# Kernel tuning notes

Measured on AMD Instinct MI355X. Metric: run time of the kernel, lower is better.

## Reference

```python
import jax, jax.numpy as jnp
import numpy as np

EMBED_DIM = 2048
HEAD_DIM = 128
BLOCK = 2048
BATCH = 8


def setup_inputs() -> dict:
    key = jax.random.key(0)
    kx, kq, kk, kv = jax.random.split(key, 4)
    x = jax.random.normal(kx, (BATCH, BLOCK, EMBED_DIM), dtype=jnp.float32)
    # torch nn.Linear(embed_dim, head_dim, bias=False) weight shape: [head_dim, embed_dim]
    s = 1.0 / np.sqrt(EMBED_DIM)
    Wq = jax.random.uniform(kq, (HEAD_DIM, EMBED_DIM), jnp.float32, -s, s)
    Wk = jax.random.uniform(kk, (HEAD_DIM, EMBED_DIM), jnp.float32, -s, s)
    Wv = jax.random.uniform(kv, (HEAD_DIM, EMBED_DIM), jnp.float32, -s, s)
    return {"x": x, "Wq": Wq, "Wk": Wk, "Wv": Wv}


def reference(x, Wq, Wk, Wv):
    B, T, C = x.shape
    # projections: y = x @ W.T
    q = jnp.einsum('btc,hc->bth', x, Wq)   # [B,T,H]
    k = jnp.einsum('btc,hc->bth', x, Wk)
    v = jnp.einsum('btc,hc->bth', x, Wv)
    # NOTE: original scales by embed_dim**0.5, not head_dim**0.5
    scale = 1.0 / jnp.sqrt(jnp.float32(C))
    logits = jnp.einsum('bth,bsh->bts', q, k) * scale  # [B,T,T]
    # causal mask (is_decoder=True)
    causal = jnp.tril(jnp.ones((T, T), dtype=bool))
    logits = jnp.where(causal, logits, -jnp.inf)
    weights = jax.nn.softmax(logits, axis=-1)
    attention = jnp.einsum('bts,bsh->bth', weights, v)  # [B,T,H]
    return attention
```

## Files before the change

### kernel.cpp

```cpp
#include <hip/hip_runtime.h>
#include <hip/hip_bf16.h>
#include <stdint.h>

constexpr int B    = 8;
constexpr int T    = 2048;
constexpr int EMB  = 2048;
constexpr int HD   = 128;
constexpr int M    = B * T;
constexpr int NW   = 3 * HD;

typedef __attribute__((ext_vector_type(8))) short short8;
typedef __attribute__((ext_vector_type(4))) float f32x4;

__device__ inline unsigned short f2bf(float f) {
    union { float f; unsigned int u; } v; v.f = f;
    unsigned int x = v.u;
    unsigned int r = (x + 0x7FFFu + ((x >> 16) & 1u)) >> 16;
    return (unsigned short)r;
}

__device__ inline unsigned int cvt_pk_bf16(float a, float b) {
    unsigned int r;
    asm volatile("v_cvt_pk_bf16_f32 %0, %1, %2" : "=v"(r) : "v"(a), "v"(b));
    return r;
}

__global__ __launch_bounds__(256) void conv_w(
    const float* __restrict__ Wq, const float* __restrict__ Wk, const float* __restrict__ Wv,
    unsigned short* __restrict__ Wb)
{
    int base = (blockIdx.x * 256 + threadIdx.x) * 8;
    int row = base >> 11, col = base & 2047;
    const float* src;
    if (row < 128)      src = Wq + (size_t)row * EMB + col;
    else if (row < 256) src = Wk + (size_t)(row - 128) * EMB + col;
    else                src = Wv + (size_t)(row - 256) * EMB + col;
    float4 a = *(const float4*)src;
    float4 b = *(const float4*)(src + 4);
    short8 sv;
    sv[0] = f2bf(a.x); sv[1] = f2bf(a.y); sv[2] = f2bf(a.z); sv[3] = f2bf(a.w);
    sv[4] = f2bf(b.x); sv[5] = f2bf(b.y); sv[6] = f2bf(b.z); sv[7] = f2bf(b.w);
    *(short8*)(Wb + base) = sv;
}

constexpr int PBM = 64;
constexpr int PBN = 192;
constexpr int PBK = 64;
constexpr int PNT = EMB / PBK;

__global__ __launch_bounds__(256, 2) void qkv_proj(
    const float* __restrict__ x, const unsigned short* __restrict__ Wb,
    unsigned short* __restrict__ Qb, unsigned short* __restrict__ Kb,
    unsigned short* __restrict__ VtG)
{
    __shared__ unsigned short Ab[2][PBM * PBK];
    __shared__ unsigned short Bb[2][PBN * PBK];

    const int d   = blockIdx.x;
    const int xcd = d & 7;
    const int g   = d >> 3;
    const int mt  = xcd * 32 + (g >> 1);
    const int ns  = g & 1;
    const int m0  = mt * PBM;
    const int n0  = ns * PBN;
    const int phase = g & 31;

    const int tid  = threadIdx.x;
    const int lane = tid & 63;
    const int w    = tid >> 6;
    const int lo   = lane & 15;
    const int hi   = lane >> 4;

    const int ar = tid >> 2;
    const int s0 = (tid & 3) * 2;
    const float* asrc = x + (size_t)(m0 + ar) * EMB + s0 * 8;

    f32x4 acc[4][3];
#pragma unroll
    for (int i = 0; i < 4; ++i)
#pragma unroll
        for (int j = 0; j < 3; ++j) acc[i][j] = (f32x4)0.0f;

    short8 breg[6];
    float4 a0, a1, a2, a3;

    auto loadTile = [&](int k0) {
#pragma unroll
        for (int it = 0; it < 6; ++it) {
            int c = it * 256 + tid;
            int row = c >> 3, seg = c & 7;
            breg[it] = *(const short8*)(Wb + (size_t)(n0 + row) * EMB + k0 + seg * 8);
        }
        a0 = *(const float4*)(asrc + k0);
        a1 = *(const float4*)(asrc + k0 + 4);
        a2 = *(const float4*)(asrc + k0 + 8);
        a3 = *(const float4*)(asrc + k0 + 12);
    };
    auto writeTile = [&](int buf) {
#pragma unroll
        for (int it = 0; it < 6; ++it) {
            int c = it * 256 + tid;
            int row = c >> 3, seg = c & 7;
            *(short8*)&Bb[buf][row * PBK + (seg ^ (row & 7)) * 8] = breg[it];
        }
        uint4 p0, p1;
        p0.x = cvt_pk_bf16(a0.x, a0.y);  p0.y = cvt_pk_bf16(a0.z, a0.w);
        p0.z = cvt_pk_bf16(a1.x, a1.y);  p0.w = cvt_pk_bf16(a1.z, a1.w);
        p1.x = cvt_pk_bf16(a2.x, a2.y);  p1.y = cvt_pk_bf16(a2.z, a2.w);
        p1.z = cvt_pk_bf16(a3.x, a3.y);  p1.w = cvt_pk_bf16(a3.z, a3.w);
        *(uint4*)&Ab[buf][ar * PBK + ((s0    ) ^ (ar & 7)) * 8] = p0;
        *(uint4*)&Ab[buf][ar * PBK + ((s0 + 1) ^ (ar & 7)) * 8] = p1;
    };
    auto compute = [&](int buf) {
#pragma unroll
        for (int kk = 0; kk < 2; ++kk) {
            short8 af[4], bf[3];
            const int cseg = kk * 4 + hi;
#pragma unroll
            for (int i = 0; i < 4; ++i) {
                int R = i * 16 + lo;
                af[i] = *(const short8*)&Ab[buf][R * PBK + (cseg ^ (R & 7)) * 8];
            }
#pragma unroll
            for (int j = 0; j < 3; ++j) {
                int n = w * 48 + j * 16 + lo;
                bf[j] = *(const short8*)&Bb[buf][n * PBK + (cseg ^ (n & 7)) * 8];
            }
#pragma unroll
            for (int i = 0; i < 4; ++i)
#pragma unroll
                for (int j = 0; j < 3; ++j)
                    acc[i][j] = __builtin_amdgcn_mfma_f32_16x16x32_bf16(af[i], bf[j], acc[i][j], 0, 0, 0);
        }
    };

    loadTile(phase * PBK);
    writeTile(0);
    __syncthreads();

#pragma unroll 1
    for (int t = 0; t < PNT; ++t) {
        const int buf = t & 1;
        if (t + 1 < PNT) {
            const int tnext = (phase + t + 1) & 31;
            loadTile(tnext * PBK);
            __builtin_amdgcn_sched_barrier(0);
        }
        compute(buf);
        if (t + 1 < PNT) {
            __builtin_amdgcn_sched_barrier(0);
            writeTile(buf ^ 1);
            __syncthreads();
        }
    }

    const int b = m0 >> 11;
#pragma unroll
    for (int i = 0; i < 4; ++i) {
        int mrow0 = m0 + i * 16 + hi * 4;
#pragma unroll
        for (int j = 0; j < 3; ++j) {
            int colbase = n0 + w * 48 + j * 16 + lo;
            if (colbase < 128) {
#pragma unroll
                for (int r = 0; r < 4; ++r)
                    Qb[(size_t)(mrow0 + r) * HD + colbase] = f2bf(acc[i][j][r]);
            } else if (colbase < 256) {
#pragma unroll
                for (int r = 0; r < 4; ++r)
                    Kb[(size_t)(mrow0 + r) * HD + (colbase - 128)] = f2bf(acc[i][j][r]);
            } else {
                int h = colbase - 256;
                int tloc = mrow0 - b * T;
                ushort4 pv;
                pv.x = f2bf(acc[i][j][0]); pv.y = f2bf(acc[i][j][1]);
                pv.z = f2bf(acc[i][j][2]); pv.w = f2bf(acc[i][j][3]);
                *(ushort4*)(VtG + ((size_t)(b * HD + h)) * T + tloc) = pv;
            }
        }
    }
}

constexpr int QB = 64;
constexpr int KB = 64;
constexpr int STILES = 8;

__global__ __launch_bounds__(256) void attn_fwd(
    const unsigned short* __restrict__ Qb,
    const unsigned short* __restrict__ Kb,
    const unsigned short* __restrict__ VtG,
    float* __restrict__ out,
    float* __restrict__ part_o, float* __restrict__ part_ml,
    int use_split)
{
    const int b  = blockIdx.y;
    int bx = blockIdx.x;
    int qt, s, nsplit;
    if (use_split) {
        if (bx < 8)       { qt = bx;               s = 0; }
        else if (bx < 24) { qt = 8  + (bx - 8) / 2;  s = (bx - 8) & 1; }
        else if (bx < 48) { qt = 16 + (bx - 24) / 3; s = (bx - 24) % 3; }
        else              { qt = 24 + (bx - 48) / 4; s = (bx - 48) & 3; }
        nsplit = qt / 8 + 1;
    } else {
        qt = bx; s = 0; nsplit = 1;
    }
    const int q0 = qt * QB;
    int t0 = s * STILES;
    int t1 = t0 + STILES; if (t1 > qt + 1) t1 = qt + 1;

    const int tid  = threadIdx.x;
    const int lane = tid & 63;
    const int w    = tid >> 6;
    const int lo   = lane & 15;
    const int hi   = lane >> 4;

    __shared__ unsigned short Ks[KB][HD + 8];
    __shared__ unsigned short Vt[HD][KB + 16];
    __shared__ unsigned short Ps[QB][KB + 8];

    short8 qf[4];
    {
        int row = q0 + w * 16 + lo;
        const unsigned short* qp = Qb + ((size_t)b * T + row) * HD + hi * 8;
#pragma unroll
        for (int ks = 0; ks < 4; ++ks) qf[ks] = *(const short8*)(qp + ks * 32);
    }

    float mrow[4], lrow[4];
    f32x4 o[8];
#pragma unroll
    for (int r = 0; r < 4; ++r) { mrow[r] = -1e30f; lrow[r] = 0.0f; }
#pragma unroll
    for (int n = 0; n < 8; ++n) o[n] = (f32x4)0.0f;

    const float scale2 = 0.022097086912079608f * 1.4426950408889634f;
    const int qrow_base = q0 + w * 16 + hi * 4;

    for (int t = t0; t < t1; ++t) {
        const int kv0 = t * KB;
#pragma unroll
        for (int it = 0; it < 4; ++it) {
            int c = tid + it * 256;
            int row = c >> 4, c8 = (c & 15) * 8;
            *(short8*)&Ks[row][c8] =
                *(const short8*)(Kb + ((size_t)b * T + kv0 + row) * HD + c8);
        }
#pragma unroll
        for (int it = 0; it < 4; ++it) {
            int c = tid + it * 256;
            int row = c >> 3, c8 = (c & 7) * 8;
            *(short8*)&Vt[row][c8] =
                *(const short8*)(VtG + (size_t)(b * HD + row) * T + kv0 + c8);
        }
        __syncthreads();

        f32x4 sa[4];
#pragma unroll
        for (int j = 0; j < 4; ++j) sa[j] = (f32x4)0.0f;
#pragma unroll
        for (int ks = 0; ks < 4; ++ks) {
#pragma unroll
            for (int j = 0; j < 4; ++j) {
                short8 bf = *(const short8*)&Ks[j * 16 + lo][ks * 32 + hi * 8];
                sa[j] = __builtin_amdgcn_mfma_f32_16x16x32_bf16(qf[ks], bf, sa[j], 0, 0, 0);
            }
        }

        const bool diag = (t == qt);
        float alpha[4];
#pragma unroll
        for (int r = 0; r < 4; ++r) {
            const int qrow = qrow_base + r;
            float rm = -1e30f;
#pragma unroll
            for (int j = 0; j < 4; ++j) {
                float v = sa[j][r] * scale2;
                if (diag) {
                    int kv = kv0 + j * 16 + lo;
                    v = (kv <= qrow) ? v : -1e30f;
                }
                sa[j][r] = v;
                rm = fmaxf(rm, v);
            }
            rm = fmaxf(rm, __shfl_xor(rm, 1));
            rm = fmaxf(rm, __shfl_xor(rm, 2));
            rm = fmaxf(rm, __shfl_xor(rm, 4));
            rm = fmaxf(rm, __shfl_xor(rm, 8));
            float mn = fmaxf(mrow[r], rm);
            alpha[r] = exp2f(mrow[r] - mn);
            mrow[r] = mn;
            float ls = 0.0f;
#pragma unroll
            for (int j = 0; j < 4; ++j) {
                float p = exp2f(sa[j][r] - mn);
                sa[j][r] = p;
                ls += p;
            }
            ls += __shfl_xor(ls, 1);
            ls += __shfl_xor(ls, 2);
            ls += __shfl_xor(ls, 4);
            ls += __shfl_xor(ls, 8);
            lrow[r] = lrow[r] * alpha[r] + ls;
        }
#pragma unroll
        for (int n = 0; n < 8; ++n)
#pragma unroll
            for (int r = 0; r < 4; ++r) o[n][r] *= alpha[r];

#pragma unroll
        for (int r = 0; r < 4; ++r)
#pragma unroll
            for (int j = 0; j < 4; ++j)
                Ps[w * 16 + hi * 4 + r][j * 16 + lo] = f2bf(sa[j][r]);
        __syncthreads();

#pragma unroll
        for (int ks = 0; ks < 2; ++ks) {
            short8 af = *(const short8*)&Ps[w * 16 + lo][ks * 32 + hi * 8];
#pragma unroll
            for (int n = 0; n < 8; ++n) {
                short8 bv = *(const short8*)&Vt[n * 16 + lo][ks * 32 + hi * 8];
                o[n] = __builtin_amdgcn_mfma_f32_16x16x32_bf16(af, bv, o[n], 0, 0, 0);
            }
        }
        __syncthreads();
    }

    if (nsplit == 1) {
#pragma unroll
        for (int n = 0; n < 8; ++n) {
            int h = n * 16 + lo;
#pragma unroll
            for (int r = 0; r < 4; ++r) {
                int row = qrow_base + r;
                out[((size_t)b * T + row) * HD + h] = o[n][r] / lrow[r];
            }
        }
    } else {
        const size_t slot = (size_t)(b * 32 + qt) * 4 + s;
        float* po = part_o + slot * (QB * HD);
#pragma unroll
        for (int n = 0; n < 8; ++n) {
            int h = n * 16 + lo;
#pragma unroll
            for (int r = 0; r < 4; ++r)
                po[(w * 16 + hi * 4 + r) * HD + h] = o[n][r];
        }
        if (lo == 0) {
            float* pm = part_ml + slot * (QB * 2);
#pragma unroll
            for (int r = 0; r < 4; ++r) {
                pm[(w * 16 + hi * 4 + r) * 2 + 0] = mrow[r];
                pm[(w * 16 + hi * 4 + r) * 2 + 1] = lrow[r];
            }
        }
    }
}

__global__ __launch_bounds__(256) void attn_combine(
    const float* __restrict__ part_o, const float* __restrict__ part_ml,
    float* __restrict__ out)
{
    const int qt = 8 + blockIdx.x;
    const int b  = blockIdx.y;
    const int ns = qt / 8 + 1;
    const int tid = threadIdx.x;
    const int row = tid >> 2;
    const int c0  = (tid & 3) * 32;
    const size_t slot0 = (size_t)(b * 32 + qt) * 4;

    float mi[4], li[4];
    float m = -1e30f;
#pragma unroll 4
    for (int i = 0; i < ns; ++i) {
        mi[i] = part_ml[(slot0 + i) * (QB * 2) + row * 2 + 0];
        li[i] = part_ml[(slot0 + i) * (QB * 2) + row * 2 + 1];
        m = fmaxf(m, mi[i]);
    }
    float L = 0.0f, f[4];
#pragma unroll 4
    for (int i = 0; i < ns; ++i) {
        f[i] = exp2f(mi[i] - m);
        L += li[i] * f[i];
    }
    const float inv = 1.0f / L;

    float4 acc[8];
#pragma unroll
    for (int k = 0; k < 8; ++k) acc[k] = make_float4(0.f, 0.f, 0.f, 0.f);
#pragma unroll 4
    for (int i = 0; i < ns; ++i) {
        const float4* src = (const float4*)(part_o + (slot0 + i) * (QB * HD) + row * HD + c0);
#pragma unroll
        for (int k = 0; k < 8; ++k) {
            float4 v = src[k];
            acc[k].x += f[i] * v.x; acc[k].y += f[i] * v.y;
            acc[k].z += f[i] * v.z; acc[k].w += f[i] * v.w;
        }
    }
    float4* dst = (float4*)(out + ((size_t)b * T + qt * QB + row) * HD + c0);
#pragma unroll
    for (int k = 0; k < 8; ++k) {
        float4 v = acc[k];
        dst[k] = make_float4(v.x * inv, v.y * inv, v.z * inv, v.w * inv);
    }
}

extern "C" void kernel_launch(void* const* d_in, const int* in_sizes, int n_in,
                              void* d_out, int out_size, void* d_ws, size_t ws_size,
                              hipStream_t stream)
{
    const float* x  = (const float*)d_in[0];
    const float* Wq = (const float*)d_in[1];
    const float* Wk = (const float*)d_in[2];
    const float* Wv = (const float*)d_in[3];
    float* out = (float*)d_out;

    const size_t off_Wb = 0;
    const size_t off_Q  = off_Wb + (size_t)NW * EMB * 2;
    const size_t off_K  = off_Q  + (size_t)M * HD * 2;
    const size_t off_V  = off_K  + (size_t)M * HD * 2;
    const size_t off_po = off_V  + (size_t)M * HD * 2;
    const size_t off_ml = off_po + (size_t)1024 * QB * HD * 4;
    const size_t total  = off_ml + (size_t)1024 * QB * 2 * 4;

    char* ws = (char*)d_ws;
    unsigned short* Wb  = (unsigned short*)(ws + off_Wb);
    unsigned short* Qb  = (unsigned short*)(ws + off_Q);
    unsigned short* Kb  = (unsigned short*)(ws + off_K);
    unsigned short* VtG = (unsigned short*)(ws + off_V);
    float* part_o  = (float*)(ws + off_po);
    float* part_ml = (float*)(ws + off_ml);

    const int use_split = (ws_size >= total) ? 1 : 0;

    conv_w<<<dim3((NW * EMB) / (256 * 8)), 256, 0, stream>>>(Wq, Wk, Wv, Wb);
    qkv_proj<<<dim3(512), 256, 0, stream>>>(x, Wb, Qb, Kb, VtG);
    attn_fwd<<<dim3(use_split ? 80 : 32, B), 256, 0, stream>>>(
        Qb, Kb, VtG, out, part_o, part_ml, use_split);
    if (use_split)
        attn_combine<<<dim3(24, B), 256, 0, stream>>>(part_o, part_ml, out);
}
```

Measured before the change: 102.1 us.

## Prefetch next K/V tile into registers and double-buffer K in shared memory

```diff
diff --git a/kernel.cpp b/kernel.cpp
--- a/kernel.cpp
+++ b/kernel.cpp
@@ -215,9 +215,37 @@
     const int lo   = lane & 15;
     const int hi   = lane >> 4;
 
-    __shared__ unsigned short Ks[KB][HD + 8];
+    __shared__ unsigned short Ks[2][KB][HD + 8];
     __shared__ unsigned short Vt[HD][KB + 16];
     __shared__ unsigned short Ps[QB][KB + 8];
+
+    short8 kreg[4], vreg[4];
+    auto issueKV = [&](int kv0) {
+#pragma unroll
+        for (int it = 0; it < 4; ++it) {
+            int c = tid + it * 256;
+            kreg[it] = *(const short8*)(Kb + ((size_t)b * T + kv0 + (c >> 4)) * HD + (c & 15) * 8);
+        }
+#pragma unroll
+        for (int it = 0; it < 4; ++it) {
+            int c = tid + it * 256;
+            vreg[it] = *(const short8*)(VtG + (size_t)(b * HD + (c >> 3)) * T + kv0 + (c & 7) * 8);
+        }
+    };
+    auto writeK = [&](int buf) {
+#pragma unroll
+        for (int it = 0; it < 4; ++it) {
+            int c = tid + it * 256;
+            *(short8*)&Ks[buf][c >> 4][(c & 15) * 8] = kreg[it];
+        }
+    };
+    auto writeV = [&]() {
+#pragma unroll
+        for (int it = 0; it < 4; ++it) {
+            int c = tid + it * 256;
+            *(short8*)&Vt[c >> 3][(c & 7) * 8] = vreg[it];
+        }
+    };
 
     short8 qf[4];
     {
@@ -237,23 +265,16 @@
     const float scale2 = 0.022097086912079608f * 1.4426950408889634f;
     const int qrow_base = q0 + w * 16 + hi * 4;
 
+    issueKV(t0 * KB);
+    writeK(0);
+    writeV();
+    __syncthreads();
+
     for (int t = t0; t < t1; ++t) {
         const int kv0 = t * KB;
-#pragma unroll
-        for (int it = 0; it < 4; ++it) {
-            int c = tid + it * 256;
-            int row = c >> 4, c8 = (c & 15) * 8;
-            *(short8*)&Ks[row][c8] =
-                *(const short8*)(Kb + ((size_t)b * T + kv0 + row) * HD + c8);
-        }
-#pragma unroll
-        for (int it = 0; it < 4; ++it) {
-            int c = tid + it * 256;
-            int row = c >> 3, c8 = (c & 7) * 8;
-            *(short8*)&Vt[row][c8] =
-                *(const short8*)(VtG + (size_t)(b * HD + row) * T + kv0 + c8);
-        }
-        __syncthreads();
+        const int buf = (t - t0) & 1;
+        const bool more = (t + 1 < t1);
+        if (more) issueKV((t + 1) * KB);
 
         f32x4 sa[4];
 #pragma unroll
@@ -262,7 +283,7 @@
         for (int ks = 0; ks < 4; ++ks) {
 #pragma unroll
             for (int j = 0; j < 4; ++j) {
-                short8 bf = *(const short8*)&Ks[j * 16 + lo][ks * 32 + hi * 8];
+                short8 bf = *(const short8*)&Ks[buf][j * 16 + lo][ks * 32 + hi * 8];
                 sa[j] = __builtin_amdgcn_mfma_f32_16x16x32_bf16(qf[ks], bf, sa[j], 0, 0, 0);
             }
         }
@@ -324,7 +345,12 @@
                 o[n] = __builtin_amdgcn_mfma_f32_16x16x32_bf16(af, bv, o[n], 0, 0, 0);
             }
         }
-        __syncthreads();
+
+        if (more) {
+            writeK(buf ^ 1);
+            __syncthreads();
+            writeV();
+        }
     }
 
     if (nsplit == 1) {
```

Result: slower. 104.2 us (+2.0%).

## Halve QKV projection N-tile for more blocks and store split partials in bf16

Applied to the files above, without the earlier changes.

```diff
diff --git a/kernel.cpp b/kernel.cpp
--- a/kernel.cpp
+++ b/kernel.cpp
@@ -17,6 +17,11 @@
     unsigned int x = v.u;
     unsigned int r = (x + 0x7FFFu + ((x >> 16) & 1u)) >> 16;
     return (unsigned short)r;
+}
+
+__device__ inline float bf2f(unsigned short s) {
+    union { unsigned int u; float f; } v; v.u = ((unsigned int)s) << 16;
+    return v.f;
 }
 
 __device__ inline unsigned int cvt_pk_bf16(float a, float b) {
@@ -44,11 +49,11 @@
 }
 
 constexpr int PBM = 64;
-constexpr int PBN = 192;
+constexpr int PBN = 96;
 constexpr int PBK = 64;
 constexpr int PNT = EMB / PBK;
 
-__global__ __launch_bounds__(256, 2) void qkv_proj(
+__global__ __launch_bounds__(256, 4) void qkv_proj(
     const float* __restrict__ x, const unsigned short* __restrict__ Wb,
     unsigned short* __restrict__ Qb, unsigned short* __restrict__ Kb,
     unsigned short* __restrict__ VtG)
@@ -59,15 +64,17 @@
     const int d   = blockIdx.x;
     const int xcd = d & 7;
     const int g   = d >> 3;
-    const int mt  = xcd * 32 + (g >> 1);
-    const int ns  = g & 1;
+    const int mt  = xcd * 32 + (g >> 2);
+    const int nq  = g & 3;
     const int m0  = mt * PBM;
-    const int n0  = ns * PBN;
+    const int n0  = nq * PBN;
     const int phase = g & 31;
 
     const int tid  = threadIdx.x;
     const int lane = tid & 63;
     const int w    = tid >> 6;
+    const int wr   = w >> 1;
+    const int wc   = w & 1;
     const int lo   = lane & 15;
     const int hi   = lane >> 4;
 
@@ -75,18 +82,18 @@
     const int s0 = (tid & 3) * 2;
     const float* asrc = x + (size_t)(m0 + ar) * EMB + s0 * 8;
 
-    f32x4 acc[4][3];
-#pragma unroll
-    for (int i = 0; i < 4; ++i)
+    f32x4 acc[2][3];
+#pragma unroll
+    for (int i = 0; i < 2; ++i)
 #pragma unroll
         for (int j = 0; j < 3; ++j) acc[i][j] = (f32x4)0.0f;
 
-    short8 breg[6];
+    short8 breg[3];
     float4 a0, a1, a2, a3;
 
     auto loadTile = [&](int k0) {
 #pragma unroll
-        for (int it = 0; it < 6; ++it) {
+        for (int it = 0; it < 3; ++it) {
             int c = it * 256 + tid;
             int row = c >> 3, seg = c & 7;
             breg[it] = *(const short8*)(Wb + (size_t)(n0 + row) * EMB + k0 + seg * 8);
@@ -98,7 +105,7 @@
     };
     auto writeTile = [&](int buf) {
 #pragma unroll
-        for (int it = 0; it < 6; ++it) {
+        for (int it = 0; it < 3; ++it) {
             int c = it * 256 + tid;
             int row = c >> 3, seg = c & 7;
             *(short8*)&Bb[buf][row * PBK + (seg ^ (row & 7)) * 8] = breg[it];
@@ -114,20 +121,20 @@
     auto compute = [&](int buf) {
 #pragma unroll
         for (int kk = 0; kk < 2; ++kk) {
-            short8 af[4], bf[3];
+            short8 af[2], bf[3];
             const int cseg = kk * 4 + hi;
 #pragma unroll
-            for (int i = 0; i < 4; ++i) {
-                int R = i * 16 + lo;
+            for (int i = 0; i < 2; ++i) {
+                int R = wr * 32 + i * 16 + lo;
                 af[i] = *(const short8*)&Ab[buf][R * PBK + (cseg ^ (R & 7)) * 8];
             }
 #pragma unroll
             for (int j = 0; j < 3; ++j) {
-                int n = w * 48 + j * 16 + lo;
+                int n = wc * 48 + j * 16 + lo;
                 bf[j] = *(const short8*)&Bb[buf][n * PBK + (cseg ^ (n & 7)) * 8];
             }
 #pragma unroll
-            for (int i = 0; i < 4; ++i)
+            for (int i = 0; i < 2; ++i)
 #pragma unroll
                 for (int j = 0; j < 3; ++j)
                     acc[i][j] = __builtin_amdgcn_mfma_f32_16x16x32_bf16(af[i], bf[j], acc[i][j], 0, 0, 0);
@@ -156,11 +163,11 @@
 
     const int b = m0 >> 11;
 #pragma unroll
-    for (int i = 0; i < 4; ++i) {
-        int mrow0 = m0 + i * 16 + hi * 4;
+    for (int i = 0; i < 2; ++i) {
+        int mrow0 = m0 + wr * 32 + i * 16 + hi * 4;
 #pragma unroll
         for (int j = 0; j < 3; ++j) {
-            int colbase = n0 + w * 48 + j * 16 + lo;
+            int colbase = n0 + wc * 48 + j * 16 + lo;
             if (colbase < 128) {
 #pragma unroll
                 for (int r = 0; r < 4; ++r)
@@ -190,7 +197,7 @@
     const unsigned short* __restrict__ Kb,
     const unsigned short* __restrict__ VtG,
     float* __restrict__ out,
-    float* __restrict__ part_o, float* __restrict__ part_ml,
+    unsigned short* __restrict__ part_o, float* __restrict__ part_ml,
     int use_split)
 {
     const int b  = blockIdx.y;
@@ -339,13 +346,13 @@
         }
     } else {
         const size_t slot = (size_t)(b * 32 + qt) * 4 + s;
-        float* po = part_o + slot * (QB * HD);
+        unsigned short* po = part_o + slot * (QB * HD);
 #pragma unroll
         for (int n = 0; n < 8; ++n) {
             int h = n * 16 + lo;
 #pragma unroll
             for (int r = 0; r < 4; ++r)
-                po[(w * 16 + hi * 4 + r) * HD + h] = o[n][r];
+                po[(w * 16 + hi * 4 + r) * HD + h] = f2bf(o[n][r]);
         }
         if (lo == 0) {
             float* pm = part_ml + slot * (QB * 2);
@@ -359,7 +366,7 @@
 }
 
 __global__ __launch_bounds__(256) void attn_combine(
-    const float* __restrict__ part_o, const float* __restrict__ part_ml,
+    const unsigned short* __restrict__ part_o, const float* __restrict__ part_ml,
     float* __restrict__ out)
 {
     const int qt = 8 + blockIdx.x;
@@ -386,25 +393,25 @@
     }
     const float inv = 1.0f / L;
 
-    float4 acc[8];
-#pragma unroll
-    for (int k = 0; k < 8; ++k) acc[k] = make_float4(0.f, 0.f, 0.f, 0.f);
+    float acc[32];
+#pragma unroll
+    for (int k = 0; k < 32; ++k) acc[k] = 0.0f;
 #pragma unroll 4
     for (int i = 0; i < ns; ++i) {
-        const float4* src = (const float4*)(part_o + (slot0 + i) * (QB * HD) + row * HD + c0);
-#pragma unroll
-        for (int k = 0; k < 8; ++k) {
-            float4 v = src[k];
-            acc[k].x += f[i] * v.x; acc[k].y += f[i] * v.y;
-            acc[k].z += f[i] * v.z; acc[k].w += f[i] * v.w;
+        const short8* src = (const short8*)(part_o + (slot0 + i) * (QB * HD) + row * HD + c0);
+#pragma unroll
+        for (int k = 0; k < 4; ++k) {
+            short8 v = src[k];
+#pragma unroll
+            for (int e = 0; e < 8; ++e)
+                acc[k * 8 + e] += f[i] * bf2f((unsigned short)v[e]);
         }
     }
     float4* dst = (float4*)(out + ((size_t)b * T + qt * QB + row) * HD + c0);
 #pragma unroll
-    for (int k = 0; k < 8; ++k) {
-        float4 v = acc[k];
-        dst[k] = make_float4(v.x * inv, v.y * inv, v.z * inv, v.w * inv);
-    }
+    for (int k = 0; k < 8; ++k)
+        dst[k] = make_float4(acc[k * 4 + 0] * inv, acc[k * 4 + 1] * inv,
+                             acc[k * 4 + 2] * inv, acc[k * 4 + 3] * inv);
 }
 
 extern "C" void kernel_launch(void* const* d_in, const int* in_sizes, int n_in,
@@ -430,13 +437,13 @@
     unsigned short* Qb  = (unsigned short*)(ws + off_Q);
     unsigned short* Kb  = (unsigned short*)(ws + off_K);
     unsigned short* VtG = (unsigned short*)(ws + off_V);
-    float* part_o  = (float*)(ws + off_po);
+    unsigned short* part_o = (unsigned short*)(ws + off_po);
     float* part_ml = (float*)(ws + off_ml);
 
     const int use_split = (ws_size >= total) ? 1 : 0;
 
     conv_w<<<dim3((NW * EMB) / (256 * 8)), 256, 0, stream>>>(Wq, Wk, Wv, Wb);
-    qkv_proj<<<dim3(512), 256, 0, stream>>>(x, Wb, Qb, Kb, VtG);
+    qkv_proj<<<dim3(1024), 256, 0, stream>>>(x, Wb, Qb, Kb, VtG);
     attn_fwd<<<dim3(use_split ? 80 : 32, B), 256, 0, stream>>>(
         Qb, Kb, VtG, out, part_o, part_ml, use_split);
     if (use_split)
```

New measurement: 116.8 us. 1.14x slower.
